# Kernel optimization log

Hardware: AMD Instinct MI355X
Metric: run time of the kernel (lower is better)

The kernel has to match this reference:

```python
import jax, jax.numpy as jnp
import numpy as np

N_NODES = 50000
N_EDGES = 800000
N_GRAPHS = 50
D_IN = 128
D_HID = 128
D_OUT = 10


def setup_inputs() -> dict:
    key = jax.random.key(0)
    ks = jax.random.split(key, 8)
    h = jax.random.normal(ks[0], (N_NODES, D_IN), dtype=jnp.float32)
    src = jax.random.randint(ks[1], (N_EDGES,), 0, N_NODES, dtype=jnp.int32)
    dst = jax.random.randint(ks[2], (N_EDGES,), 0, N_NODES, dtype=jnp.int32)
    graph_ids = jnp.sort(jax.random.randint(ks[3], (N_NODES,), 0, N_GRAPHS, dtype=jnp.int32))
    s = 1.0 / np.sqrt(D_HID)
    W1 = jax.random.normal(ks[4], (D_IN, D_HID), dtype=jnp.float32) * s
    W2 = jax.random.normal(ks[5], (D_HID, D_HID), dtype=jnp.float32) * s
    W3 = jax.random.normal(ks[6], (D_HID, D_HID), dtype=jnp.float32) * s
    Wm = jax.random.normal(ks[7], (D_HID, D_OUT), dtype=jnp.float32) * s
    return {
        "h": h, "src": src, "dst": dst, "graph_ids": graph_ids,
        "W1": W1, "b1": jnp.zeros((D_HID,), jnp.float32),
        "W2": W2, "b2": jnp.zeros((D_HID,), jnp.float32),
        "W3": W3, "b3": jnp.zeros((D_HID,), jnp.float32),
        "Wm": Wm, "bm": jnp.zeros((D_OUT,), jnp.float32),
    }


def _graph_conv(h, W, b, src, dst, norm_src, norm_dst):
    # DGL GraphConv, norm='both': out = D_dst^{-1/2} * A @ (D_src^{-1/2} * h) @ W + b
    m = (h * norm_src[:, None])[src]              # [E, d] gather (memory-bound)
    agg = jax.ops.segment_sum(m, dst, num_segments=N_NODES)  # [N, d] scatter-add
    return (agg * norm_dst[:, None]) @ W + b


def reference(h, src, dst, graph_ids, W1, b1, W2, b2, W3, b3, Wm, bm):
    ones_e = jnp.ones((N_EDGES,), jnp.float32)
    out_deg = jax.ops.segment_sum(ones_e, src, num_segments=N_NODES)
    in_deg = jax.ops.segment_sum(ones_e, dst, num_segments=N_NODES)
    norm_src = jnp.clip(out_deg, 1.0, None) ** -0.5
    norm_dst = jnp.clip(in_deg, 1.0, None) ** -0.5

    h = jax.nn.relu(_graph_conv(h, W1, b1, src, dst, norm_src, norm_dst))
    h = jax.nn.relu(_graph_conv(h, W2, b2, src, dst, norm_src, norm_dst))
    h = jax.nn.relu(_graph_conv(h, W3, b3, src, dst, norm_src, norm_dst))

    # mean-nodes readout per graph
    hg_sum = jax.ops.segment_sum(h, graph_ids, num_segments=N_GRAPHS)  # [G, d]
    cnt = jax.ops.segment_sum(jnp.ones((N_NODES,), jnp.float32), graph_ids, num_segments=N_GRAPHS)
    hg = hg_sum / jnp.clip(cnt, 1.0, None)[:, None]

    logits = hg @ Wm + bm                                 # [G, D_OUT]
    return jax.nn.log_softmax(logits, axis=0)             # faithful to dim=0 in source
```

## Files before the change

### kernel.cpp

```cpp
#include <hip/hip_runtime.h>

#define N_NODES 50000
#define N_EDGES 800000
#define N_GRAPHS 50
#define D 128
#define D_OUT 10
#define PLANE_F4 200000

__global__ __launch_bounds__(256) void hist_edges(const int* __restrict__ src,
                                                  const int* __restrict__ dst,
                                                  int* __restrict__ cnt_dst,
                                                  int* __restrict__ cnt_src) {
    int i = blockIdx.x * 256 + threadIdx.x;
    if (i < N_EDGES) {
        atomicAdd(&cnt_dst[dst[i]], 1);
        atomicAdd(&cnt_src[src[i]], 1);
    }
}

__global__ __launch_bounds__(1024) void scan_k(int* __restrict__ cnt,
                                               int* __restrict__ row_ptr) {
    __shared__ int wsum[16];
    __shared__ int carry_s;
    int tid = threadIdx.x;
    int lane = tid & 63, wid = tid >> 6;
    if (tid == 0) carry_s = 0;
    __syncthreads();
    for (int base = 0; base < N_NODES; base += 4096) {
        int i0 = base + tid * 4;
        int v0 = (i0 + 0 < N_NODES) ? cnt[i0 + 0] : 0;
        int v1 = (i0 + 1 < N_NODES) ? cnt[i0 + 1] : 0;
        int v2 = (i0 + 2 < N_NODES) ? cnt[i0 + 2] : 0;
        int v3 = (i0 + 3 < N_NODES) ? cnt[i0 + 3] : 0;
        int s = v0 + v1 + v2 + v3;
        int x = s;
        #pragma unroll
        for (int d = 1; d < 64; d <<= 1) {
            int y = __shfl_up(x, d, 64);
            if (lane >= d) x += y;
        }
        if (lane == 63) wsum[wid] = x;
        __syncthreads();
        if (wid == 0) {
            int t = (lane < 16) ? wsum[lane] : 0;
            #pragma unroll
            for (int d = 1; d < 16; d <<= 1) {
                int y = __shfl_up(t, d, 64);
                if (lane >= d) t += y;
            }
            if (lane < 16) wsum[lane] = t;
        }
        __syncthreads();
        int woff = (wid == 0) ? 0 : wsum[wid - 1];
        int excl = carry_s + woff + (x - s);
        int run = excl;
        if (i0 + 0 < N_NODES) { row_ptr[i0 + 0] = run; cnt[i0 + 0] = run; } run += v0;
        if (i0 + 1 < N_NODES) { row_ptr[i0 + 1] = run; cnt[i0 + 1] = run; } run += v1;
        if (i0 + 2 < N_NODES) { row_ptr[i0 + 2] = run; cnt[i0 + 2] = run; } run += v2;
        if (i0 + 3 < N_NODES) { row_ptr[i0 + 3] = run; cnt[i0 + 3] = run; } run += v3;
        __syncthreads();
        if (tid == 0) carry_s += wsum[15];
        __syncthreads();
    }
    if (tid == 0) row_ptr[N_NODES] = carry_s;
}

__global__ __launch_bounds__(256) void norms_k(const int* __restrict__ cnt_src,
                                               const int* __restrict__ row_ptr,
                                               float* __restrict__ ns,
                                               float* __restrict__ nd) {
    int v = blockIdx.x * 256 + threadIdx.x;
    if (v < N_NODES) {
        int od = cnt_src[v];
        int id = row_ptr[v + 1] - row_ptr[v];
        ns[v] = 1.0f / sqrtf((float)(od > 1 ? od : 1));
        nd[v] = 1.0f / sqrtf((float)(id > 1 ? id : 1));
    }
}

__global__ __launch_bounds__(256) void scatter_k(const int* __restrict__ src,
                                                 const int* __restrict__ dst,
                                                 int* __restrict__ fill,
                                                 unsigned short* __restrict__ col) {
    int i = blockIdx.x * 256 + threadIdx.x;
    if (i < N_EDGES) {
        int s = src[i];
        int d = dst[i];
        int p = atomicAdd(&fill[d], 1);
        col[p] = (unsigned short)s;
    }
}

__global__ __launch_bounds__(256) void prescale_k(const float* __restrict__ h,
                                                  const float* __restrict__ ns,
                                                  float* __restrict__ out) {
    int i = blockIdx.x * 256 + threadIdx.x;
    if (i < N_NODES * 32) {
        int node = i >> 5;
        int kg = i & 31;
        float4 v = ((const float4*)h)[i];
        float s = ns[node];
        int p = kg >> 2, q = kg & 3;
        ((float4*)out)[p * PLANE_F4 + node * 4 + q] =
            make_float4(v.x * s, v.y * s, v.z * s, v.w * s);
    }
}

__global__ __launch_bounds__(256) void spmm_k(const float* __restrict__ x,
                                              const int* __restrict__ row_ptr,
                                              const unsigned short* __restrict__ col,
                                              const float* __restrict__ nd,
                                              float* __restrict__ out) {
    int b = blockIdx.x;
    int slice = b & 7;
    int node = (b >> 3) * 64 + (threadIdx.x >> 2);
    if (node >= N_NODES) return;
    int q = threadIdx.x & 3;
    int s = row_ptr[node];
    int e = row_ptr[node + 1];
    const float4* xp = (const float4*)x + slice * PLANE_F4;
    float4 a0 = make_float4(0.f, 0.f, 0.f, 0.f);
    float4 a1 = make_float4(0.f, 0.f, 0.f, 0.f);
    int i = s;
    for (; i + 4 <= e; i += 4) {
        int c0 = col[i], c1 = col[i + 1], c2 = col[i + 2], c3 = col[i + 3];
        float4 h0 = xp[c0 * 4 + q];
        float4 h1 = xp[c1 * 4 + q];
        float4 h2 = xp[c2 * 4 + q];
        float4 h3 = xp[c3 * 4 + q];
        a0.x += h0.x; a0.y += h0.y; a0.z += h0.z; a0.w += h0.w;
        a1.x += h1.x; a1.y += h1.y; a1.z += h1.z; a1.w += h1.w;
        a0.x += h2.x; a0.y += h2.y; a0.z += h2.z; a0.w += h2.w;
        a1.x += h3.x; a1.y += h3.y; a1.z += h3.z; a1.w += h3.w;
    }
    for (; i < e; i++) {
        float4 hv = xp[col[i] * 4 + q];
        a0.x += hv.x; a0.y += hv.y; a0.z += hv.z; a0.w += hv.w;
    }
    float ndv = nd[node];
    ((float4*)out)[slice * PLANE_F4 + node * 4 + q] =
        make_float4((a0.x + a1.x) * ndv, (a0.y + a1.y) * ndv,
                    (a0.z + a1.z) * ndv, (a0.w + a1.w) * ndv);
}

template <int MODE>
__global__ __launch_bounds__(256) void gemm_relu_k(const float* __restrict__ A,
                                                   const float* __restrict__ W,
                                                   const float* __restrict__ bias,
                                                   const float* __restrict__ ns,
                                                   float* __restrict__ out) {
    __shared__ float As_t[128 * 64];
    __shared__ float Ws[128 * 64];
    int tid = threadIdx.x;
    int row0 = blockIdx.x * 64;
    const float4* A4 = (const float4*)A;

    #pragma unroll
    for (int it = 0; it < 8; it++) {
        int linear = it * 256 + tid;
        int p = linear >> 8;
        int rem = linear & 255;
        int r = rem >> 2;
        int q = rem & 3;
        int row = row0 + r;
        float4 a = (row < N_NODES) ? A4[p * PLANE_F4 + row * 4 + q]
                                   : make_float4(0.f, 0.f, 0.f, 0.f);
        int kb = p * 16 + q * 4;
        As_t[(kb + 0) * 64 + r] = a.x;
        As_t[(kb + 1) * 64 + r] = a.y;
        As_t[(kb + 2) * 64 + r] = a.z;
        As_t[(kb + 3) * 64 + r] = a.w;
    }

    int cg = tid & 15;
    int rg = tid >> 4;
    float acc[2][4][4];
    #pragma unroll
    for (int h = 0; h < 2; h++)
        #pragma unroll
        for (int r = 0; r < 4; r++)
            #pragma unroll
            for (int c = 0; c < 4; c++) acc[h][r][c] = 0.f;

    for (int h = 0; h < 2; h++) {
        __syncthreads();
        #pragma unroll
        for (int it = 0; it < 8; it++) {
            int linear = it * 256 + tid;
            int k = linear >> 4;
            int c4 = linear & 15;
            ((float4*)Ws)[linear] = ((const float4*)(W + k * 128 + h * 64))[c4];
        }
        __syncthreads();
        float (*ah)[4] = acc[h];
        for (int k = 0; k < 128; k++) {
            float4 av = *(const float4*)(As_t + k * 64 + rg * 4);
            float4 wv = *(const float4*)(Ws + k * 64 + cg * 4);
            ah[0][0] = fmaf(av.x, wv.x, ah[0][0]);
            ah[0][1] = fmaf(av.x, wv.y, ah[0][1]);
            ah[0][2] = fmaf(av.x, wv.z, ah[0][2]);
            ah[0][3] = fmaf(av.x, wv.w, ah[0][3]);
            ah[1][0] = fmaf(av.y, wv.x, ah[1][0]);
            ah[1][1] = fmaf(av.y, wv.y, ah[1][1]);
            ah[1][2] = fmaf(av.y, wv.z, ah[1][2]);
            ah[1][3] = fmaf(av.y, wv.w, ah[1][3]);
            ah[2][0] = fmaf(av.z, wv.x, ah[2][0]);
            ah[2][1] = fmaf(av.z, wv.y, ah[2][1]);
            ah[2][2] = fmaf(av.z, wv.z, ah[2][2]);
            ah[2][3] = fmaf(av.z, wv.w, ah[2][3]);
            ah[3][0] = fmaf(av.w, wv.x, ah[3][0]);
            ah[3][1] = fmaf(av.w, wv.y, ah[3][1]);
            ah[3][2] = fmaf(av.w, wv.z, ah[3][2]);
            ah[3][3] = fmaf(av.w, wv.w, ah[3][3]);
        }
    }

    #pragma unroll
    for (int h = 0; h < 2; h++) {
        float4 bv = ((const float4*)bias)[h * 16 + cg];
        #pragma unroll
        for (int r = 0; r < 4; r++) {
            int row = row0 + rg * 4 + r;
            if (row < N_NODES) {
                float4 o;
                o.x = fmaxf(acc[h][r][0] + bv.x, 0.f);
                o.y = fmaxf(acc[h][r][1] + bv.y, 0.f);
                o.z = fmaxf(acc[h][r][2] + bv.z, 0.f);
                o.w = fmaxf(acc[h][r][3] + bv.w, 0.f);
                if (MODE == 0) {
                    float s = ns[row];
                    o.x *= s; o.y *= s; o.z *= s; o.w *= s;
                    int p = h * 4 + (cg >> 2);
                    int q = cg & 3;
                    ((float4*)out)[p * PLANE_F4 + row * 4 + q] = o;
                } else {
                    ((float4*)out)[row * 32 + h * 16 + cg] = o;
                }
            }
        }
    }
}

__global__ __launch_bounds__(256) void proj_readout_k(const float* __restrict__ h,
                                                      const int* __restrict__ gid,
                                                      const float* __restrict__ Wm,
                                                      float* __restrict__ hgp,
                                                      int* __restrict__ gcnt) {
    __shared__ float Wmt[10 * 144];
    int tid = threadIdx.x;
    for (int i = tid; i < 1280; i += 256) {
        int k = i / 10, o = i % 10;
        Wmt[o * 144 + k + 4 * (k >> 5)] = Wm[i];
    }
    __syncthreads();

    int v = blockIdx.x * 64 + (tid >> 2);
    int quarter = tid & 3;
    int lane = tid & 63;

    float acc[D_OUT];
    #pragma unroll
    for (int o = 0; o < D_OUT; o++) acc[o] = 0.f;
    int g = -1;
    int cnt = 0;
    if (v < N_NODES) {
        g = gid[v];
        cnt = (quarter == 0) ? 1 : 0;
        const float4* h4 = (const float4*)h + v * 32 + quarter * 8;
        const float* wbase = Wmt + quarter * 36;
        #pragma unroll
        for (int kk = 0; kk < 8; kk++) {
            float4 hv = h4[kk];
            #pragma unroll
            for (int o = 0; o < D_OUT; o++) {
                float4 w = *(const float4*)(wbase + o * 144 + kk * 4);
                acc[o] += hv.x * w.x + hv.y * w.y + hv.z * w.z + hv.w * w.w;
            }
        }
    }

    #pragma unroll
    for (int d = 1; d < 64; d <<= 1) {
        int gp = __shfl_up(g, d, 64);
        int cp = __shfl_up(cnt, d, 64);
        bool take = (lane >= d) && (gp == g);
        #pragma unroll
        for (int o = 0; o < D_OUT; o++) {
            float ap = __shfl_up(acc[o], d, 64);
            if (take) acc[o] += ap;
        }
        if (take) cnt += cp;
    }
    int gn = __shfl_down(g, 1, 64);
    bool tail = (lane == 63) || (gn != g);
    if (tail && g >= 0) {
        #pragma unroll
        for (int o = 0; o < D_OUT; o++) atomicAdd(&hgp[g * D_OUT + o], acc[o]);
        if (cnt > 0) atomicAdd(&gcnt[g], cnt);
    }
}

__global__ __launch_bounds__(512) void final_k(const float* __restrict__ hgp,
                                               const int* __restrict__ gcnt,
                                               const float* __restrict__ bm,
                                               float* __restrict__ out) {
    __shared__ float lg[N_GRAPHS * D_OUT];
    __shared__ float colm[D_OUT], colls[D_OUT];
    int tid = threadIdx.x;
    if (tid < N_GRAPHS * D_OUT) {
        int g = tid / D_OUT, o = tid % D_OUT;
        float c = (float)gcnt[g];
        lg[tid] = hgp[tid] / (c > 1.f ? c : 1.f) + bm[o];
    }
    __syncthreads();
    if (tid < D_OUT) {
        float m = -1e30f;
        for (int g = 0; g < N_GRAPHS; g++) m = fmaxf(m, lg[g * D_OUT + tid]);
        float s = 0.f;
        for (int g = 0; g < N_GRAPHS; g++) s += expf(lg[g * D_OUT + tid] - m);
        colm[tid] = m; colls[tid] = logf(s);
    }
    __syncthreads();
    if (tid < N_GRAPHS * D_OUT) {
        int o = tid % D_OUT;
        out[tid] = lg[tid] - colm[o] - colls[o];
    }
}

extern "C" void kernel_launch(void* const* d_in, const int* in_sizes, int n_in,
                              void* d_out, int out_size, void* d_ws, size_t ws_size,
                              hipStream_t stream) {
    const float* h_in = (const float*)d_in[0];
    const int*   src  = (const int*)d_in[1];
    const int*   dst  = (const int*)d_in[2];
    const int*   gid  = (const int*)d_in[3];
    const float* W1 = (const float*)d_in[4];  const float* b1 = (const float*)d_in[5];
    const float* W2 = (const float*)d_in[6];  const float* b2 = (const float*)d_in[7];
    const float* W3 = (const float*)d_in[8];  const float* b3 = (const float*)d_in[9];
    const float* Wm = (const float*)d_in[10]; const float* bm = (const float*)d_in[11];

    char* ws = (char*)d_ws;
    int*            cnt     = (int*)(ws + 0);
    int*            cnt_src = (int*)(ws + 200000);
    int*            gcnt    = (int*)(ws + 400000);
    float*          hgp     = (float*)(ws + 400256);
    int*            row_ptr = (int*)(ws + 402304);
    unsigned short* col16   = (unsigned short*)(ws + 602320);
    float*          ns      = (float*)(ws + 2202320);
    float*          nd      = (float*)(ws + 2402320);
    float*          bufA    = (float*)(ws + 2602320);
    float*          bufB    = (float*)(ws + 28202320);

    hipMemsetAsync(ws, 0, 402304, stream);

    hist_edges<<<3125, 256, 0, stream>>>(src, dst, cnt, cnt_src);
    scan_k<<<1, 1024, 0, stream>>>(cnt, row_ptr);
    norms_k<<<196, 256, 0, stream>>>(cnt_src, row_ptr, ns, nd);
    scatter_k<<<3125, 256, 0, stream>>>(src, dst, cnt, col16);
    prescale_k<<<6250, 256, 0, stream>>>(h_in, ns, bufA);

    spmm_k<<<6256, 256, 0, stream>>>(bufA, row_ptr, col16, nd, bufB);
    gemm_relu_k<0><<<782, 256, 0, stream>>>(bufB, W1, b1, ns, bufA);
    spmm_k<<<6256, 256, 0, stream>>>(bufA, row_ptr, col16, nd, bufB);
    gemm_relu_k<0><<<782, 256, 0, stream>>>(bufB, W2, b2, ns, bufA);
    spmm_k<<<6256, 256, 0, stream>>>(bufA, row_ptr, col16, nd, bufB);
    gemm_relu_k<1><<<782, 256, 0, stream>>>(bufB, W3, b3, ns, bufA);

    proj_readout_k<<<782, 256, 0, stream>>>(bufA, gid, Wm, hgp, gcnt);
    final_k<<<1, 512, 0, stream>>>(hgp, gcnt, bm, (float*)d_out);
}
```

Before: 536.1 us.

## Shard degree histograms, parallelize CSR scan, and enlarge GEMM tiles

The edge-degree histogram and CSR scatter now spread their atomics over 8 shard copies of the counters to reduce contention. The single-block serial scan is replaced by a three-kernel multi-block scan that also computes the norms. The dense GEMM now uses 256-row tiles with an 8x8 register tile per thread and reads W directly from global memory instead of shared memory. In exchange this adds more kernel launches and uses 128 KB of LDS per GEMM block, which limits occupancy and leaves only 196 blocks.

```diff
diff --git a/kernel.cpp b/kernel.cpp
--- a/kernel.cpp
+++ b/kernel.cpp
@@ -6,87 +6,110 @@
 #define D 128
 #define D_OUT 10
 #define PLANE_F4 200000
-
-__global__ __launch_bounds__(256) void hist_edges(const int* __restrict__ src,
-                                                  const int* __restrict__ dst,
-                                                  int* __restrict__ cnt_dst,
-                                                  int* __restrict__ cnt_src) {
+#define NSH 8
+
+__global__ __launch_bounds__(256) void hist8_k(const int* __restrict__ src,
+                                               const int* __restrict__ dst,
+                                               int* __restrict__ cnt8,
+                                               int* __restrict__ cs8) {
     int i = blockIdx.x * 256 + threadIdx.x;
+    int sh = (blockIdx.x & (NSH - 1)) * N_NODES;
     if (i < N_EDGES) {
-        atomicAdd(&cnt_dst[dst[i]], 1);
-        atomicAdd(&cnt_src[src[i]], 1);
-    }
-}
-
-__global__ __launch_bounds__(1024) void scan_k(int* __restrict__ cnt,
-                                               int* __restrict__ row_ptr) {
-    __shared__ int wsum[16];
-    __shared__ int carry_s;
-    int tid = threadIdx.x;
-    int lane = tid & 63, wid = tid >> 6;
-    if (tid == 0) carry_s = 0;
-    __syncthreads();
-    for (int base = 0; base < N_NODES; base += 4096) {
-        int i0 = base + tid * 4;
-        int v0 = (i0 + 0 < N_NODES) ? cnt[i0 + 0] : 0;
-        int v1 = (i0 + 1 < N_NODES) ? cnt[i0 + 1] : 0;
-        int v2 = (i0 + 2 < N_NODES) ? cnt[i0 + 2] : 0;
-        int v3 = (i0 + 3 < N_NODES) ? cnt[i0 + 3] : 0;
-        int s = v0 + v1 + v2 + v3;
-        int x = s;
-        #pragma unroll
-        for (int d = 1; d < 64; d <<= 1) {
-            int y = __shfl_up(x, d, 64);
-            if (lane >= d) x += y;
-        }
-        if (lane == 63) wsum[wid] = x;
-        __syncthreads();
-        if (wid == 0) {
-            int t = (lane < 16) ? wsum[lane] : 0;
-            #pragma unroll
-            for (int d = 1; d < 16; d <<= 1) {
-                int y = __shfl_up(t, d, 64);
-                if (lane >= d) t += y;
-            }
-            if (lane < 16) wsum[lane] = t;
-        }
-        __syncthreads();
-        int woff = (wid == 0) ? 0 : wsum[wid - 1];
-        int excl = carry_s + woff + (x - s);
-        int run = excl;
-        if (i0 + 0 < N_NODES) { row_ptr[i0 + 0] = run; cnt[i0 + 0] = run; } run += v0;
-        if (i0 + 1 < N_NODES) { row_ptr[i0 + 1] = run; cnt[i0 + 1] = run; } run += v1;
-        if (i0 + 2 < N_NODES) { row_ptr[i0 + 2] = run; cnt[i0 + 2] = run; } run += v2;
-        if (i0 + 3 < N_NODES) { row_ptr[i0 + 3] = run; cnt[i0 + 3] = run; } run += v3;
-        __syncthreads();
-        if (tid == 0) carry_s += wsum[15];
-        __syncthreads();
-    }
-    if (tid == 0) row_ptr[N_NODES] = carry_s;
-}
-
-__global__ __launch_bounds__(256) void norms_k(const int* __restrict__ cnt_src,
-                                               const int* __restrict__ row_ptr,
+        atomicAdd(&cnt8[sh + dst[i]], 1);
+        atomicAdd(&cs8[sh + src[i]], 1);
+    }
+}
+
+__global__ __launch_bounds__(256) void scanA_k(const int* __restrict__ cnt8,
+                                               int* __restrict__ bs) {
+    int b = blockIdx.x, t = threadIdx.x;
+    int n = b * 196 + t;
+    int v = 0;
+    if (t < 196 && n < N_NODES) {
+        #pragma unroll
+        for (int x = 0; x < NSH; x++) v += cnt8[x * N_NODES + n];
+    }
+    __shared__ int wsum[4];
+    int lane = t & 63, wid = t >> 6;
+    #pragma unroll
+    for (int d = 32; d; d >>= 1) v += __shfl_down(v, d, 64);
+    if (lane == 0) wsum[wid] = v;
+    __syncthreads();
+    if (t == 0) bs[b] = wsum[0] + wsum[1] + wsum[2] + wsum[3];
+}
+
+__global__ __launch_bounds__(256) void scanB_k(int* __restrict__ bs) {
+    int t = threadIdx.x;
+    int v = bs[t];
+    int lane = t & 63, wid = t >> 6;
+    __shared__ int wsum[4];
+    int x = v;
+    #pragma unroll
+    for (int d = 1; d < 64; d <<= 1) {
+        int y = __shfl_up(x, d, 64);
+        if (lane >= d) x += y;
+    }
+    if (lane == 63) wsum[wid] = x;
+    __syncthreads();
+    int add = 0;
+    #pragma unroll
+    for (int i = 0; i < 4; i++) if (i < wid) add += wsum[i];
+    bs[t] = add + x - v;
+}
+
+__global__ __launch_bounds__(256) void scanC_k(int* __restrict__ cnt8,
+                                               const int* __restrict__ cs8,
+                                               const int* __restrict__ bs,
+                                               int* __restrict__ row_ptr,
                                                float* __restrict__ ns,
                                                float* __restrict__ nd) {
-    int v = blockIdx.x * 256 + threadIdx.x;
-    if (v < N_NODES) {
-        int od = cnt_src[v];
-        int id = row_ptr[v + 1] - row_ptr[v];
-        ns[v] = 1.0f / sqrtf((float)(od > 1 ? od : 1));
-        nd[v] = 1.0f / sqrtf((float)(id > 1 ? id : 1));
-    }
-}
-
-__global__ __launch_bounds__(256) void scatter_k(const int* __restrict__ src,
-                                                 const int* __restrict__ dst,
-                                                 int* __restrict__ fill,
-                                                 unsigned short* __restrict__ col) {
+    int b = blockIdx.x, t = threadIdx.x;
+    int n = b * 196 + t;
+    bool act = (t < 196) && (n < N_NODES);
+    int c[NSH];
+    int v = 0;
+    if (act) {
+        #pragma unroll
+        for (int x = 0; x < NSH; x++) { c[x] = cnt8[x * N_NODES + n]; v += c[x]; }
+    }
+    int lane = t & 63, wid = t >> 6;
+    __shared__ int wsum[4];
+    int xv = v;
+    #pragma unroll
+    for (int d = 1; d < 64; d <<= 1) {
+        int y = __shfl_up(xv, d, 64);
+        if (lane >= d) xv += y;
+    }
+    if (lane == 63) wsum[wid] = xv;
+    __syncthreads();
+    int add = 0;
+    #pragma unroll
+    for (int i = 0; i < 4; i++) if (i < wid) add += wsum[i];
+    int excl = bs[b] + add + xv - v;
+    if (act) {
+        row_ptr[n] = excl;
+        int rb = excl;
+        #pragma unroll
+        for (int x = 0; x < NSH; x++) { cnt8[x * N_NODES + n] = rb; rb += c[x]; }
+        int od = 0;
+        #pragma unroll
+        for (int x = 0; x < NSH; x++) od += cs8[x * N_NODES + n];
+        ns[n] = 1.0f / sqrtf((float)(od > 1 ? od : 1));
+        nd[n] = 1.0f / sqrtf((float)(v > 1 ? v : 1));
+    }
+    if (b == 255 && t == 0) row_ptr[N_NODES] = N_EDGES;
+}
+
+__global__ __launch_bounds__(256) void scatter8_k(const int* __restrict__ src,
+                                                  const int* __restrict__ dst,
+                                                  int* __restrict__ cursor8,
+                                                  unsigned short* __restrict__ col) {
     int i = blockIdx.x * 256 + threadIdx.x;
+    int sh = (blockIdx.x & (NSH - 1)) * N_NODES;
     if (i < N_EDGES) {
         int s = src[i];
         int d = dst[i];
-        int p = atomicAdd(&fill[d], 1);
+        int p = atomicAdd(&cursor8[sh + d], 1);
         col[p] = (unsigned short)s;
     }
 }
@@ -144,98 +167,84 @@
 }
 
 template <int MODE>
-__global__ __launch_bounds__(256) void gemm_relu_k(const float* __restrict__ A,
+__global__ __launch_bounds__(512) void gemm_relu_k(const float* __restrict__ A,
                                                    const float* __restrict__ W,
                                                    const float* __restrict__ bias,
                                                    const float* __restrict__ ns,
                                                    float* __restrict__ out) {
-    __shared__ float As_t[128 * 64];
-    __shared__ float Ws[128 * 64];
+    __shared__ float As_t[128 * 256];
     int tid = threadIdx.x;
-    int row0 = blockIdx.x * 64;
+    int row0 = blockIdx.x * 256;
     const float4* A4 = (const float4*)A;
 
     #pragma unroll
-    for (int it = 0; it < 8; it++) {
-        int linear = it * 256 + tid;
-        int p = linear >> 8;
-        int rem = linear & 255;
+    for (int it = 0; it < 16; it++) {
+        int linear = it * 512 + tid;
+        int p = linear >> 10;
+        int rem = linear & 1023;
         int r = rem >> 2;
         int q = rem & 3;
         int row = row0 + r;
         float4 a = (row < N_NODES) ? A4[p * PLANE_F4 + row * 4 + q]
                                    : make_float4(0.f, 0.f, 0.f, 0.f);
         int kb = p * 16 + q * 4;
-        As_t[(kb + 0) * 64 + r] = a.x;
-        As_t[(kb + 1) * 64 + r] = a.y;
-        As_t[(kb + 2) * 64 + r] = a.z;
-        As_t[(kb + 3) * 64 + r] = a.w;
-    }
-
-    int cg = tid & 15;
-    int rg = tid >> 4;
-    float acc[2][4][4];
-    #pragma unroll
-    for (int h = 0; h < 2; h++)
-        #pragma unroll
-        for (int r = 0; r < 4; r++)
+        As_t[(kb + 0) * 256 + r] = a.x;
+        As_t[(kb + 1) * 256 + r] = a.y;
+        As_t[(kb + 2) * 256 + r] = a.z;
+        As_t[(kb + 3) * 256 + r] = a.w;
+    }
+    __syncthreads();
+
+    int tc = tid & 15;
+    int tr = tid >> 4;
+    float acc[8][8];
+    #pragma unroll
+    for (int r = 0; r < 8; r++)
+        #pragma unroll
+        for (int c = 0; c < 8; c++) acc[r][c] = 0.f;
+
+    const float4* W4 = (const float4*)W;
+    #pragma unroll 2
+    for (int k = 0; k < 128; k++) {
+        float4 w0 = W4[k * 32 + tc * 2];
+        float4 w1 = W4[k * 32 + tc * 2 + 1];
+        float4 a0 = *(const float4*)(As_t + k * 256 + tr * 8);
+        float4 a1 = *(const float4*)(As_t + k * 256 + tr * 8 + 4);
+        float av[8] = {a0.x, a0.y, a0.z, a0.w, a1.x, a1.y, a1.z, a1.w};
+        float wv[8] = {w0.x, w0.y, w0.z, w0.w, w1.x, w1.y, w1.z, w1.w};
+        #pragma unroll
+        for (int rr = 0; rr < 8; rr++)
             #pragma unroll
-            for (int c = 0; c < 4; c++) acc[h][r][c] = 0.f;
-
-    for (int h = 0; h < 2; h++) {
-        __syncthreads();
-        #pragma unroll
-        for (int it = 0; it < 8; it++) {
-            int linear = it * 256 + tid;
-            int k = linear >> 4;
-            int c4 = linear & 15;
-            ((float4*)Ws)[linear] = ((const float4*)(W + k * 128 + h * 64))[c4];
-        }
-        __syncthreads();
-        float (*ah)[4] = acc[h];
-        for (int k = 0; k < 128; k++) {
-            float4 av = *(const float4*)(As_t + k * 64 + rg * 4);
-            float4 wv = *(const float4*)(Ws + k * 64 + cg * 4);
-            ah[0][0] = fmaf(av.x, wv.x, ah[0][0]);
-            ah[0][1] = fmaf(av.x, wv.y, ah[0][1]);
-            ah[0][2] = fmaf(av.x, wv.z, ah[0][2]);
-            ah[0][3] = fmaf(av.x, wv.w, ah[0][3]);
-            ah[1][0] = fmaf(av.y, wv.x, ah[1][0]);
-            ah[1][1] = fmaf(av.y, wv.y, ah[1][1]);
-            ah[1][2] = fmaf(av.y, wv.z, ah[1][2]);
-            ah[1][3] = fmaf(av.y, wv.w, ah[1][3]);
-            ah[2][0] = fmaf(av.z, wv.x, ah[2][0]);
-            ah[2][1] = fmaf(av.z, wv.y, ah[2][1]);
-            ah[2][2] = fmaf(av.z, wv.z, ah[2][2]);
-            ah[2][3] = fmaf(av.z, wv.w, ah[2][3]);
-            ah[3][0] = fmaf(av.w, wv.x, ah[3][0]);
-            ah[3][1] = fmaf(av.w, wv.y, ah[3][1]);
-            ah[3][2] = fmaf(av.w, wv.z, ah[3][2]);
-            ah[3][3] = fmaf(av.w, wv.w, ah[3][3]);
-        }
-    }
-
-    #pragma unroll
-    for (int h = 0; h < 2; h++) {
-        float4 bv = ((const float4*)bias)[h * 16 + cg];
-        #pragma unroll
-        for (int r = 0; r < 4; r++) {
-            int row = row0 + rg * 4 + r;
-            if (row < N_NODES) {
-                float4 o;
-                o.x = fmaxf(acc[h][r][0] + bv.x, 0.f);
-                o.y = fmaxf(acc[h][r][1] + bv.y, 0.f);
-                o.z = fmaxf(acc[h][r][2] + bv.z, 0.f);
-                o.w = fmaxf(acc[h][r][3] + bv.w, 0.f);
-                if (MODE == 0) {
-                    float s = ns[row];
-                    o.x *= s; o.y *= s; o.z *= s; o.w *= s;
-                    int p = h * 4 + (cg >> 2);
-                    int q = cg & 3;
-                    ((float4*)out)[p * PLANE_F4 + row * 4 + q] = o;
-                } else {
-                    ((float4*)out)[row * 32 + h * 16 + cg] = o;
-                }
+            for (int cc = 0; cc < 8; cc++)
+                acc[rr][cc] = fmaf(av[rr], wv[cc], acc[rr][cc]);
+    }
+
+    float4 bv0 = ((const float4*)bias)[tc * 2];
+    float4 bv1 = ((const float4*)bias)[tc * 2 + 1];
+    #pragma unroll
+    for (int rr = 0; rr < 8; rr++) {
+        int row = row0 + tr * 8 + rr;
+        if (row < N_NODES) {
+            float4 o0, o1;
+            o0.x = fmaxf(acc[rr][0] + bv0.x, 0.f);
+            o0.y = fmaxf(acc[rr][1] + bv0.y, 0.f);
+            o0.z = fmaxf(acc[rr][2] + bv0.z, 0.f);
+            o0.w = fmaxf(acc[rr][3] + bv0.w, 0.f);
+            o1.x = fmaxf(acc[rr][4] + bv1.x, 0.f);
+            o1.y = fmaxf(acc[rr][5] + bv1.y, 0.f);
+            o1.z = fmaxf(acc[rr][6] + bv1.z, 0.f);
+            o1.w = fmaxf(acc[rr][7] + bv1.w, 0.f);
+            if (MODE == 0) {
+                float s = ns[row];
+                o0.x *= s; o0.y *= s; o0.z *= s; o0.w *= s;
+                o1.x *= s; o1.y *= s; o1.z *= s; o1.w *= s;
+                int p = tc >> 1;
+                int q0 = (tc & 1) * 2;
+                ((float4*)out)[p * PLANE_F4 + row * 4 + q0] = o0;
+                ((float4*)out)[p * PLANE_F4 + row * 4 + q0 + 1] = o1;
+            } else {
+                ((float4*)out)[row * 32 + tc * 2] = o0;
+                ((float4*)out)[row * 32 + tc * 2 + 1] = o1;
             }
         }
     }
@@ -340,31 +349,35 @@
     const float* Wm = (const float*)d_in[10]; const float* bm = (const float*)d_in[11];
 
     char* ws = (char*)d_ws;
-    int*            cnt     = (int*)(ws + 0);
-    int*            cnt_src = (int*)(ws + 200000);
-    int*            gcnt    = (int*)(ws + 400000);
-    float*          hgp     = (float*)(ws + 400256);
-    int*            row_ptr = (int*)(ws + 402304);
-    unsigned short* col16   = (unsigned short*)(ws + 602320);
-    float*          ns      = (float*)(ws + 2202320);
-    float*          nd      = (float*)(ws + 2402320);
-    float*          bufA    = (float*)(ws + 2602320);
-    float*          bufB    = (float*)(ws + 28202320);
-
-    hipMemsetAsync(ws, 0, 402304, stream);
-
-    hist_edges<<<3125, 256, 0, stream>>>(src, dst, cnt, cnt_src);
-    scan_k<<<1, 1024, 0, stream>>>(cnt, row_ptr);
-    norms_k<<<196, 256, 0, stream>>>(cnt_src, row_ptr, ns, nd);
-    scatter_k<<<3125, 256, 0, stream>>>(src, dst, cnt, col16);
+    int*            row_ptr = (int*)(ws + 0);
+    unsigned short* col16   = (unsigned short*)(ws + 200032);
+    float*          ns      = (float*)(ws + 1800032);
+    float*          nd      = (float*)(ws + 2000032);
+    int*            gcnt    = (int*)(ws + 2200032);
+    float*          hgp     = (float*)(ws + 2200288);
+    int*            bs      = (int*)(ws + 2202336);
+    float*          bufA    = (float*)(ws + 2203360);
+    float*          bufB    = (float*)(ws + 27803360);
+    int*            cnt8    = (int*)bufA;
+    int*            cs8     = (int*)bufB;
+
+    hipMemsetAsync(ws + 2200032, 0, 2304, stream);
+    hipMemsetAsync(cnt8, 0, 1600000, stream);
+    hipMemsetAsync(cs8, 0, 1600000, stream);
+
+    hist8_k<<<3125, 256, 0, stream>>>(src, dst, cnt8, cs8);
+    scanA_k<<<256, 256, 0, stream>>>(cnt8, bs);
+    scanB_k<<<1, 256, 0, stream>>>(bs);
+    scanC_k<<<256, 256, 0, stream>>>(cnt8, cs8, bs, row_ptr, ns, nd);
+    scatter8_k<<<3125, 256, 0, stream>>>(src, dst, cnt8, col16);
     prescale_k<<<6250, 256, 0, stream>>>(h_in, ns, bufA);
 
     spmm_k<<<6256, 256, 0, stream>>>(bufA, row_ptr, col16, nd, bufB);
-    gemm_relu_k<0><<<782, 256, 0, stream>>>(bufB, W1, b1, ns, bufA);
+    gemm_relu_k<0><<<196, 512, 0, stream>>>(bufB, W1, b1, ns, bufA);
     spmm_k<<<6256, 256, 0, stream>>>(bufA, row_ptr, col16, nd, bufB);
-    gemm_relu_k<0><<<782, 256, 0, stream>>>(bufB, W2, b2, ns, bufA);
+    gemm_relu_k<0><<<196, 512, 0, stream>>>(bufB, W2, b2, ns, bufA);
     spmm_k<<<6256, 256, 0, stream>>>(bufA, row_ptr, col16, nd, bufB);
-    gemm_relu_k<1><<<782, 256, 0, stream>>>(bufB, W3, b3, ns, bufA);
+    gemm_relu_k<1><<<196, 512, 0, stream>>>(bufB, W3, b3, ns, bufA);
 
     proj_readout_k<<<782, 256, 0, stream>>>(bufA, gid, Wm, hgp, gcnt);
     final_k<<<1, 512, 0, stream>>>(hgp, gcnt, bm, (float*)d_out);
```

After: 523.2 us. 2.4% less time.
